# Kernel optimization log

Hardware: AMD Instinct MI355X
Metric: run time of the kernel (lower is better)

## Reference

```python
import jax, jax.numpy as jnp
import numpy as np

# Dimensions chosen per init_kwargs / input_specs
B, INC, OUTC, H, W = 16, 512, 256, 32, 32
FD = H * W           # flattened_dim = 1024 (perfect square)
DK = INC // 4        # 128, projection dim of the rotatory attention
EPS_BN = 1e-5


def setup_inputs() -> dict:
    key = jax.random.key(0)
    ks = jax.random.split(key, 8)
    sc = lambda fan_in: 1.0 / np.sqrt(fan_in)
    return {
        "x": jax.random.normal(ks[0], (B, INC, H, W), jnp.float32),
        "s": jax.random.normal(ks[1], (B, OUTC, 2 * H, 2 * W), jnp.float32),
        # ConvTranspose2d(inc, outc, 2, 2): torch weight shape (in, out, kH, kW)
        "up_w": jax.random.normal(ks[2], (INC, OUTC, 2, 2), jnp.float32) * sc(INC * 4),
        "up_b": jnp.zeros((OUTC,), jnp.float32),
        # LinearRotatoryAttentionModule projections: Linear(flattened_dim, inc//4) x3
        "wq": jax.random.normal(ks[3], (FD, DK), jnp.float32) * sc(FD),
        "wkl": jax.random.normal(ks[4], (FD, DK), jnp.float32) * sc(FD),
        "wkr": jax.random.normal(ks[5], (FD, DK), jnp.float32) * sc(FD),
        # conv_block(2*outc, outc): Conv2d 3x3 pad 1 + BatchNorm + ReLU
        "c1_w": jax.random.normal(ks[6], (OUTC, 2 * OUTC, 3, 3), jnp.float32) * sc(2 * OUTC * 9),
        "c1_b": jnp.zeros((OUTC,), jnp.float32),
        "bn_g": jnp.ones((OUTC,), jnp.float32),
        "bn_b": jnp.zeros((OUTC,), jnp.float32),
    }


def _rotatory(l, x, r, wq, wkl, wkr):
    """Linear rotatory attention on one triplet of slices, each (INC, FD).
    Center queries left and right contexts via elu+1 linear attention."""
    phi = lambda t: jax.nn.elu(t) + 1.0
    q = phi(x @ wq)        # (N, Dk)
    kl = phi(l @ wkl)      # (N, Dk)
    kr = phi(r @ wkr)      # (N, Dk)

    def linattn(k, v):
        kv = jnp.einsum('nk,nd->kd', k, v)      # (Dk, D)
        z = q @ k.sum(0) + 1e-6                  # (N,)
        return (q @ kv) / z[:, None]             # (N, D)

    return x + linattn(kl, l) + linattn(kr, r)


def reference(x, s, up_w, up_b, wq, wkl, wkr, c1_w, c1_b, bn_g, bn_b):
    # --- rotatory attention over interior batch samples (vectorized, no Python loop) ---
    xf = x.reshape(B, INC, FD)
    mid = jax.vmap(_rotatory, in_axes=(0, 0, 0, None, None, None))(
        xf[:-2], xf[1:-1], xf[2:], wq, wkl, wkr)          # (B-2, INC, FD)
    new = jnp.concatenate([x[:1], mid.reshape(B - 2, INC, H, W), x[-1:]], axis=0)

    # --- ConvTranspose2d k=2 s=2: non-overlapping, exact as einsum + reshape ---
    up = jnp.einsum('ncij,coab->noiajb', new, up_w).reshape(B, OUTC, 2 * H, 2 * W)
    up = up + up_b[None, :, None, None]

    # --- fused gate: sigmoid(relu(up + s)), then channel concat with skip ---
    g = jax.nn.sigmoid(jax.nn.relu(up + s))
    cat = jnp.concatenate([g, s], axis=1)                  # (B, 2*OUTC, 2H, 2W)

    # --- conv_block: Conv 3x3 same + BatchNorm (batch stats) + ReLU ---
    y = jax.lax.conv_general_dilated(cat, c1_w, (1, 1), 'SAME',
                                     dimension_numbers=('NCHW', 'OIHW', 'NCHW'))
    y = y + c1_b[None, :, None, None]
    mu = y.mean(axis=(0, 2, 3), keepdims=True)
    var = y.var(axis=(0, 2, 3), keepdims=True)
    y = (y - mu) / jnp.sqrt(var + EPS_BN)
    y = y * bn_g[None, :, None, None] + bn_b[None, :, None, None]
    return jax.nn.relu(y)
```

## Files before the change

### kernel.cpp

```cpp
#include <hip/hip_runtime.h>
#include <math.h>

#define B_ 16
#define INC 512
#define OUTC 256
#define FD 1024
#define DK 128
#define T_ 14
#define HO 64
#define WO 64
#define SP (HO*WO)
#define KC5P 40

typedef unsigned short u16;
typedef __attribute__((ext_vector_type(8))) short shortx8;
typedef __attribute__((ext_vector_type(4))) float floatx4;

__device__ __forceinline__ float phi_f(float t) {
    return t > 0.0f ? t + 1.0f : expf(t);
}
__device__ __forceinline__ u16 f2bf(float f) {
    unsigned int u = __float_as_uint(f);
    unsigned int r = (u + 0x7fffu + ((u >> 16) & 1u)) >> 16;
    return (u16)r;
}
__device__ __forceinline__ float bf2f(u16 h) {
    return __uint_as_float(((unsigned int)h) << 16);
}

__global__ __launch_bounds__(256) void kprep_x(const float* __restrict__ x, u16* __restrict__ xT) {
    __shared__ u16 T[64][65];
    int d0 = blockIdx.x * 64, c0 = blockIdx.y * 64, b = blockIdx.z;
    const float* src = x + (size_t)b * INC * FD;
    int tid = threadIdx.x, lr = tid >> 6, lc = tid & 63;
    #pragma unroll
    for (int i = 0; i < 16; ++i) {
        int c = lr + i * 4;
        T[lc][c] = f2bf(src[(size_t)(c0 + c) * FD + d0 + lc]);
    }
    __syncthreads();
    u16* dst = xT + (size_t)b * FD * INC;
    #pragma unroll
    for (int i = 0; i < 16; ++i) {
        int d = lr + i * 4;
        dst[(size_t)(d0 + d) * INC + c0 + lc] = T[d][lc];
    }
}

__global__ __launch_bounds__(256) void ktr_w(const float* __restrict__ src, u16* __restrict__ dst,
                                             int R, int C) {
    __shared__ u16 T[64][65];
    int c0 = blockIdx.x * 64, r0 = blockIdx.y * 64;
    int tid = threadIdx.x, lr = tid >> 6, lc = tid & 63;
    #pragma unroll
    for (int i = 0; i < 16; ++i) {
        int r = lr + i * 4;
        T[lc][r] = f2bf(src[(size_t)(r0 + r) * C + c0 + lc]);
    }
    __syncthreads();
    #pragma unroll
    for (int i = 0; i < 16; ++i) {
        int c = lr + i * 4;
        dst[(size_t)(c0 + c) * R + r0 + lc] = T[c][lc];
    }
}

__global__ void kw_tr(const float* __restrict__ c1_w, u16* __restrict__ Wt) {
    int i = blockIdx.x * 256 + threadIdx.x;
    if (i >= 256 * 512 * 9) return;
    int tap = i % 9; int t2 = i / 9;
    int c = t2 % 512; int o = t2 / 512;
    Wt[((size_t)tap * 256 + o) * 512 + c] = f2bf(c1_w[i]);
}

__global__ __launch_bounds__(256) void kborder(u16* __restrict__ P) {
    int b = blockIdx.y;
    int cbase = blockIdx.x * 20;
    uint4 z = {0, 0, 0, 0};
    for (int i = threadIdx.x; i < 20 * 64; i += 256) {
        int c = cbase + (i >> 6);
        int sub = i & 63;
        int row, col;
        if (c < 66)       { row = 0;       col = c; }
        else if (c < 132) { row = 65;      col = c - 66; }
        else if (c < 196) { row = c - 131; col = 0; }
        else              { row = c - 195; col = 65; }
        *(uint4*)(P + ((size_t)(b * 66 + row) * 66 + col) * 512 + sub * 8) = z;
    }
}

__global__ __launch_bounds__(256) void k1_proj(const float* __restrict__ x,
        const u16* __restrict__ wqT, const u16* __restrict__ wklT, const u16* __restrict__ wkrT,
        u16* __restrict__ qb, u16* __restrict__ klt, u16* __restrict__ krt) {
    __shared__ u16 smem[8704];
    u16* As = smem;
    u16* Bs = smem + 5120;
    int z = blockIdx.z, t = z / 3, which = z - t * 3;
    int src = (which == 0) ? t + 1 : (which == 1 ? t : t + 2);
    const float* Af = x + (size_t)src * INC * FD;
    const u16* Bw = (which == 0) ? wqT : (which == 1 ? wklT : wkrT);
    int n0 = blockIdx.x * 64, m0 = blockIdx.y * 128;
    int tid = threadIdx.x, w = tid >> 6, lane = tid & 63, l15 = lane & 15, quad = lane >> 4;
    int sm = tid >> 2, sq = (tid & 3) * 8;
    floatx4 acc[2][4];
    #pragma unroll
    for (int i = 0; i < 2; ++i)
        #pragma unroll
        for (int j = 0; j < 4; ++j) acc[i][j] = (floatx4){0.f,0.f,0.f,0.f};

    for (int k0 = 0; k0 < FD; k0 += 32) {
        float4 v0 = *(const float4*)&Af[(size_t)(m0 + sm) * FD + k0 + sq];
        float4 v1 = *(const float4*)&Af[(size_t)(m0 + sm) * FD + k0 + sq + 4];
        float4 v2 = *(const float4*)&Af[(size_t)(m0 + 64 + sm) * FD + k0 + sq];
        float4 v3 = *(const float4*)&Af[(size_t)(m0 + 64 + sm) * FD + k0 + sq + 4];
        union { u16 h[8]; uint4 v; } p0, p1;
        p0.h[0]=f2bf(v0.x); p0.h[1]=f2bf(v0.y); p0.h[2]=f2bf(v0.z); p0.h[3]=f2bf(v0.w);
        p0.h[4]=f2bf(v1.x); p0.h[5]=f2bf(v1.y); p0.h[6]=f2bf(v1.z); p0.h[7]=f2bf(v1.w);
        p1.h[0]=f2bf(v2.x); p1.h[1]=f2bf(v2.y); p1.h[2]=f2bf(v2.z); p1.h[3]=f2bf(v2.w);
        p1.h[4]=f2bf(v3.x); p1.h[5]=f2bf(v3.y); p1.h[6]=f2bf(v3.z); p1.h[7]=f2bf(v3.w);
        *(uint4*)&As[sm * 40 + sq] = p0.v;
        *(uint4*)&As[(64 + sm) * 40 + sq] = p1.v;
        *(uint4*)&Bs[sm * 40 + sq] = *(const uint4*)&Bw[(size_t)(n0 + sm) * FD + k0 + sq];
        __syncthreads();
        shortx8 bfr[4];
        #pragma unroll
        for (int nt = 0; nt < 4; ++nt)
            bfr[nt] = *(const shortx8*)&Bs[(nt * 16 + l15) * 40 + quad * 8];
        #pragma unroll
        for (int mt = 0; mt < 2; ++mt) {
            shortx8 af = *(const shortx8*)&As[(w * 32 + mt * 16 + l15) * 40 + quad * 8];
            #pragma unroll
            for (int nt = 0; nt < 4; ++nt)
                acc[mt][nt] = __builtin_amdgcn_mfma_f32_16x16x32_bf16(af, bfr[nt], acc[mt][nt], 0, 0, 0);
        }
        __syncthreads();
    }
    if (which == 0) {
        u16* outp = qb + (size_t)t * INC * DK;
        #pragma unroll
        for (int mt = 0; mt < 2; ++mt)
            #pragma unroll
            for (int nt = 0; nt < 4; ++nt)
                #pragma unroll
                for (int r = 0; r < 4; ++r) {
                    int m_out = m0 + w * 32 + mt * 16 + quad * 4 + r;
                    int n_out = n0 + nt * 16 + l15;
                    outp[(size_t)m_out * DK + n_out] = f2bf(phi_f(acc[mt][nt][r]));
                }
    } else {
        u16* outp = ((which == 1) ? klt : krt) + (size_t)t * DK * INC;
        #pragma unroll
        for (int mt = 0; mt < 2; ++mt)
            #pragma unroll
            for (int nt = 0; nt < 4; ++nt)
                #pragma unroll
                for (int r = 0; r < 4; ++r) {
                    int mloc = w * 32 + mt * 16 + quad * 4 + r;
                    int nloc = nt * 16 + l15;
                    smem[nloc * 136 + mloc] = f2bf(phi_f(acc[mt][nt][r]));
                }
        __syncthreads();
        int dkl = tid >> 2, seg = tid & 3;
        const uint4* sp = (const uint4*)&smem[dkl * 136 + seg * 32];
        uint4* dp = (uint4*)&outp[(size_t)(n0 + dkl) * INC + m0 + seg * 32];
        dp[0] = sp[0]; dp[1] = sp[1]; dp[2] = sp[2]; dp[3] = sp[3];
    }
}

__global__ __launch_bounds__(128) void k2b_ksum(const u16* __restrict__ klt, const u16* __restrict__ krt,
                         float* __restrict__ ksuml, float* __restrict__ ksumr) {
    int t = blockIdx.x, nb = blockIdx.y;
    int dk = threadIdx.x;
    const u16* pl = klt + ((size_t)t * DK + dk) * INC + nb * 64;
    const u16* pr = krt + ((size_t)t * DK + dk) * INC + nb * 64;
    float s1 = 0.f, s2 = 0.f;
    #pragma unroll
    for (int i = 0; i < 8; ++i) {
        union { uint4 v; u16 h[8]; } a, b;
        a.v = *(const uint4*)(pl + i * 8);
        b.v = *(const uint4*)(pr + i * 8);
        #pragma unroll
        for (int e = 0; e < 8; ++e) { s1 += bf2f(a.h[e]); s2 += bf2f(b.h[e]); }
    }
    atomicAdd(&ksuml[t * DK + dk], s1);
    atomicAdd(&ksumr[t * DK + dk], s2);
}

__global__ __launch_bounds__(512) void k2c_z(const u16* __restrict__ qb, const float* __restrict__ ksuml,
                      const float* __restrict__ ksumr, float* __restrict__ zl, float* __restrict__ zr) {
    int t = blockIdx.x; int n = threadIdx.x;
    const uint4* qp = (const uint4*)(qb + ((size_t)t * INC + n) * DK);
    const float* sl = ksuml + t * DK;
    const float* sr = ksumr + t * DK;
    float a = 0.f, b = 0.f;
    #pragma unroll
    for (int k16 = 0; k16 < 16; ++k16) {
        union { uint4 v; u16 h[8]; } q;
        q.v = qp[k16];
        #pragma unroll
        for (int e = 0; e < 8; ++e) {
            float qv = bf2f(q.h[e]);
            a = fmaf(qv, sl[k16 * 8 + e], a);
            b = fmaf(qv, sr[k16 * 8 + e], b);
        }
    }
    zl[t * INC + n] = a + 1e-6f;
    zr[t * INC + n] = b + 1e-6f;
}

__global__ __launch_bounds__(256) void k2_kv(const u16* __restrict__ xT,
        const u16* __restrict__ klt, const u16* __restrict__ krt,
        u16* __restrict__ kvlT, u16* __restrict__ kvrT) {
    __shared__ u16 As[128 * 40];
    __shared__ u16 Bs[64 * 40];
    int z = blockIdx.z, t = z >> 1, side = z & 1;
    const u16* A = xT + (size_t)(side ? t + 2 : t) * FD * INC;
    const u16* Bw = (side ? krt : klt) + (size_t)t * DK * INC;
    u16* outp = (side ? kvrT : kvlT) + (size_t)t * FD * DK;
    int n0 = blockIdx.x * 64, m0 = blockIdx.y * 128;
    int tid = threadIdx.x, w = tid >> 6, lane = tid & 63, l15 = lane & 15, quad = lane >> 4;
    int sm = tid >> 2, sq = (tid & 3) * 8;
    floatx4 acc[2][4];
    #pragma unroll
    for (int i = 0; i < 2; ++i)
        #pragma unroll
        for (int j = 0; j < 4; ++j) acc[i][j] = (floatx4){0.f,0.f,0.f,0.f};
    for (int k0 = 0; k0 < INC; k0 += 32) {
        *(uint4*)&As[sm * 40 + sq] = *(const uint4*)&A[(size_t)(m0 + sm) * INC + k0 + sq];
        *(uint4*)&As[(64 + sm) * 40 + sq] = *(const uint4*)&A[(size_t)(m0 + 64 + sm) * INC + k0 + sq];
        *(uint4*)&Bs[sm * 40 + sq] = *(const uint4*)&Bw[(size_t)(n0 + sm) * INC + k0 + sq];
        __syncthreads();
        shortx8 bfr[4];
        #pragma unroll
        for (int nt = 0; nt < 4; ++nt)
            bfr[nt] = *(const shortx8*)&Bs[(nt * 16 + l15) * 40 + quad * 8];
        #pragma unroll
        for (int mt = 0; mt < 2; ++mt) {
            shortx8 af = *(const shortx8*)&As[(w * 32 + mt * 16 + l15) * 40 + quad * 8];
            #pragma unroll
            for (int nt = 0; nt < 4; ++nt)
                acc[mt][nt] = __builtin_amdgcn_mfma_f32_16x16x32_bf16(af, bfr[nt], acc[mt][nt], 0, 0, 0);
        }
        __syncthreads();
    }
    #pragma unroll
    for (int mt = 0; mt < 2; ++mt)
        #pragma unroll
        for (int nt = 0; nt < 4; ++nt)
            #pragma unroll
            for (int r = 0; r < 4; ++r) {
                int m_out = m0 + w * 32 + mt * 16 + quad * 4 + r;
                int n_out = n0 + nt * 16 + l15;
                outp[(size_t)m_out * DK + n_out] = f2bf(acc[mt][nt][r]);
            }
}

__global__ __launch_bounds__(256) void k3_out(const u16* __restrict__ xT,
        const u16* __restrict__ qb, const u16* __restrict__ kvlT, const u16* __restrict__ kvrT,
        const float* __restrict__ zl, const float* __restrict__ zr, u16* __restrict__ newT) {
    __shared__ u16 As1[128 * 40];
    __shared__ u16 As2[128 * 40];
    __shared__ u16 Bs[64 * 40];
    int t = blockIdx.z;
    const u16* A1 = kvlT + (size_t)t * FD * DK;
    const u16* A2 = kvrT + (size_t)t * FD * DK;
    const u16* Bq = qb + (size_t)t * INC * DK;
    int n0 = blockIdx.x * 64, m0 = blockIdx.y * 128;
    int tid = threadIdx.x, w = tid >> 6, lane = tid & 63, l15 = lane & 15, quad = lane >> 4;
    int sm = tid >> 2, sq = (tid & 3) * 8;
    floatx4 accl[2][4], accr[2][4];
    #pragma unroll
    for (int i = 0; i < 2; ++i)
        #pragma unroll
        for (int j = 0; j < 4; ++j) {
            accl[i][j] = (floatx4){0.f,0.f,0.f,0.f};
            accr[i][j] = (floatx4){0.f,0.f,0.f,0.f};
        }
    for (int k0 = 0; k0 < DK; k0 += 32) {
        *(uint4*)&As1[sm * 40 + sq] = *(const uint4*)&A1[(size_t)(m0 + sm) * DK + k0 + sq];
        *(uint4*)&As1[(64 + sm) * 40 + sq] = *(const uint4*)&A1[(size_t)(m0 + 64 + sm) * DK + k0 + sq];
        *(uint4*)&As2[sm * 40 + sq] = *(const uint4*)&A2[(size_t)(m0 + sm) * DK + k0 + sq];
        *(uint4*)&As2[(64 + sm) * 40 + sq] = *(const uint4*)&A2[(size_t)(m0 + 64 + sm) * DK + k0 + sq];
        *(uint4*)&Bs[sm * 40 + sq] = *(const uint4*)&Bq[(size_t)(n0 + sm) * DK + k0 + sq];
        __syncthreads();
        shortx8 bfr[4];
        #pragma unroll
        for (int nt = 0; nt < 4; ++nt)
            bfr[nt] = *(const shortx8*)&Bs[(nt * 16 + l15) * 40 + quad * 8];
        #pragma unroll
        for (int mt = 0; mt < 2; ++mt) {
            shortx8 afl = *(const shortx8*)&As1[(w * 32 + mt * 16 + l15) * 40 + quad * 8];
            shortx8 afr = *(const shortx8*)&As2[(w * 32 + mt * 16 + l15) * 40 + quad * 8];
            #pragma unroll
            for (int nt = 0; nt < 4; ++nt) {
                accl[mt][nt] = __builtin_amdgcn_mfma_f32_16x16x32_bf16(afl, bfr[nt], accl[mt][nt], 0, 0, 0);
                accr[mt][nt] = __builtin_amdgcn_mfma_f32_16x16x32_bf16(afr, bfr[nt], accr[mt][nt], 0, 0, 0);
            }
        }
        __syncthreads();
    }
    float il[4], ir[4];
    #pragma unroll
    for (int nt = 0; nt < 4; ++nt) {
        int n_out = n0 + nt * 16 + l15;
        il[nt] = 1.0f / zl[t * INC + n_out];
        ir[nt] = 1.0f / zr[t * INC + n_out];
    }
    const u16* xc = xT + (size_t)(t + 1) * FD * INC;
    u16* outp = newT + (size_t)t * FD * INC;
    #pragma unroll
    for (int mt = 0; mt < 2; ++mt)
        #pragma unroll
        for (int nt = 0; nt < 4; ++nt)
            #pragma unroll
            for (int r = 0; r < 4; ++r) {
                int m_out = m0 + w * 32 + mt * 16 + quad * 4 + r;
                int n_out = n0 + nt * 16 + l15;
                float xv = bf2f(xc[(size_t)m_out * INC + n_out]);
                float v = xv + accl[mt][nt][r] * il[nt] + accr[mt][nt][r] * ir[nt];
                outp[(size_t)m_out * INC + n_out] = f2bf(v);
            }
}

__global__ __launch_bounds__(256) void k4_up(const u16* __restrict__ xT,
        const u16* __restrict__ newT, const u16* __restrict__ upwT,
        const float* __restrict__ up_b, u16* __restrict__ P) {
    __shared__ u16 smem[12288];
    u16* As = smem;
    u16* Bs = smem + 5120;
    int b = blockIdx.z;
    const u16* A = (b == 0) ? xT
                 : (b == B_ - 1) ? (xT + (size_t)(B_ - 1) * FD * INC)
                 : (newT + (size_t)(b - 1) * FD * INC);
    int n0 = blockIdx.x * 64, m0 = blockIdx.y * 128;
    int tid = threadIdx.x, w = tid >> 6, lane = tid & 63, l15 = lane & 15, quad = lane >> 4;
    int sm = tid >> 2, sq = (tid & 3) * 8;
    floatx4 acc[2][4];
    #pragma unroll
    for (int i = 0; i < 2; ++i)
        #pragma unroll
        for (int j = 0; j < 4; ++j) acc[i][j] = (floatx4){0.f,0.f,0.f,0.f};
    for (int k0 = 0; k0 < INC; k0 += 32) {
        *(uint4*)&As[sm * 40 + sq] = *(const uint4*)&A[(size_t)(m0 + sm) * INC + k0 + sq];
        *(uint4*)&As[(64 + sm) * 40 + sq] = *(const uint4*)&A[(size_t)(m0 + 64 + sm) * INC + k0 + sq];
        *(uint4*)&Bs[sm * 40 + sq] = *(const uint4*)&upwT[(size_t)(n0 + sm) * INC + k0 + sq];
        __syncthreads();
        shortx8 bfr[4];
        #pragma unroll
        for (int nt = 0; nt < 4; ++nt)
            bfr[nt] = *(const shortx8*)&Bs[(nt * 16 + l15) * 40 + quad * 8];
        #pragma unroll
        for (int mt = 0; mt < 2; ++mt) {
            shortx8 af = *(const shortx8*)&As[(w * 32 + mt * 16 + l15) * 40 + quad * 8];
            #pragma unroll
            for (int nt = 0; nt < 4; ++nt)
                acc[mt][nt] = __builtin_amdgcn_mfma_f32_16x16x32_bf16(af, bfr[nt], acc[mt][nt], 0, 0, 0);
        }
        __syncthreads();
    }
    u16* Ts = smem;
    int ppos = (l15 & 3) * 128;
    #pragma unroll
    for (int mt = 0; mt < 2; ++mt)
        #pragma unroll
        for (int nt = 0; nt < 4; ++nt) {
            int lm = nt * 16 + l15;
            float bias = up_b[(n0 + lm) >> 2];
            int o_rel = lm >> 2;
            #pragma unroll
            for (int r = 0; r < 4; ++r) {
                int l = w * 32 + mt * 16 + quad * 4 + r;
                Ts[(ppos + l) * 24 + o_rel] = f2bf(acc[mt][nt][r] + bias);
            }
        }
    __syncthreads();
    #pragma unroll
    for (int j2 = 0; j2 < 2; ++j2) {
        int pi = tid + j2 * 256;
        int pp = pi >> 7, l = pi & 127;
        int aa = pp >> 1, cbb = pp & 1;
        int px = m0 + l;
        int row = 2 * (px >> 5) + aa, colq = 2 * (px & 31) + cbb;
        size_t dst = ((size_t)(b * 66 + 1 + row) * 66 + 1 + colq) * 512 + (n0 >> 2);
        union { uint4 v; u16 h[8]; } a0, a1, s0, s1, g0, g1;
        a0.v = *(const uint4*)&Ts[pi * 24];
        a1.v = *(const uint4*)&Ts[pi * 24 + 8];
        s0.v = *(const uint4*)(P + dst + 256);
        s1.v = *(const uint4*)(P + dst + 256 + 8);
        #pragma unroll
        for (int e = 0; e < 8; ++e) {
            float r0 = fmaxf(bf2f(a0.h[e]) + bf2f(s0.h[e]), 0.0f);
            float r1 = fmaxf(bf2f(a1.h[e]) + bf2f(s1.h[e]), 0.0f);
            g0.h[e] = f2bf(1.0f / (1.0f + expf(-r0)));
            g1.h[e] = f2bf(1.0f / (1.0f + expf(-r1)));
        }
        *(uint4*)(P + dst) = g0.v;
        *(uint4*)(P + dst + 8) = g1.v;
    }
}

__global__ __launch_bounds__(256) void k4b_sfill(const float* __restrict__ s_in,
                                                 u16* __restrict__ P) {
    __shared__ u16 T[64 * 264];
    int p = blockIdx.x;
    int b = blockIdx.y;
    int tid = threadIdx.x;
    int qcol = tid & 63;
    int ob = tid >> 6;
    for (int o = ob; o < 256; o += 4) {
        float v = s_in[((size_t)(b * OUTC + o) * HO + p) * WO + qcol];
        T[qcol * 264 + o] = f2bf(v);
    }
    __syncthreads();
    int q2 = tid >> 2;
    int sg = tid & 3;
    size_t base = ((size_t)(b * 66 + 1 + p) * 66 + 1 + q2) * 512 + 256;
    #pragma unroll
    for (int it = 0; it < 8; ++it) {
        int seg = sg + it * 4;
        uint4 v = *(const uint4*)&T[q2 * 264 + seg * 8];
        *(uint4*)(P + base + seg * 8) = v;
    }
}

__global__ __launch_bounds__(256) void k5_mfma(const u16* __restrict__ P,
        const u16* __restrict__ Wt, const float* __restrict__ c1_b,
        float* __restrict__ y) {
    __shared__ u16 Xs[6 * 66 * KC5P];
    int rb = blockIdx.x;
    int o0 = blockIdx.y * 64;
    int b  = blockIdx.z;
    int tid = threadIdx.x;
    int w = tid >> 6, lane = tid & 63;
    int l15 = lane & 15, quad = lane >> 4;

    floatx4 acc[4][4];
    #pragma unroll
    for (int i = 0; i < 4; ++i)
        #pragma unroll
        for (int j = 0; j < 4; ++j)
            acc[i][j] = (floatx4){0.f, 0.f, 0.f, 0.f};

    size_t Pbase = ((size_t)b * 66 + (size_t)rb * 4) * 66 * 512;
    const u16* Wbase = Wt + ((size_t)o0 + (size_t)l15) * 512 + quad * 8;

    for (int ch = 0; ch < 16; ++ch) {
        int c0 = ch * 32;
        __syncthreads();
        #pragma unroll
        for (int it = 0; it < 8; ++it) {
            int s = it * 256 + tid;
            if (s < 1980) {
                int pix = s / 5;
                int cs = s - pix * 5;
                int csel = (cs == 4) ? 0 : cs;
                const u16* gp = P + Pbase + (size_t)pix * 512 + c0 + csel * 8;
                __builtin_amdgcn_global_load_lds(
                    (const __attribute__((address_space(1))) void*)gp,
                    (__attribute__((address_space(3))) void*)&Xs[(size_t)(it * 256 + w * 64) * 8],
                    16, 0, 0);
            }
        }
        __syncthreads();
        shortx8 wfb[2][4];
        #pragma unroll
        for (int nt = 0; nt < 4; ++nt)
            wfb[0][nt] = *(const shortx8*)(Wbase + ((size_t)nt * 16) * 512 + c0);
        #pragma unroll
        for (int tap = 0; tap < 9; ++tap) {
            if (tap < 8) {
                #pragma unroll
                for (int nt = 0; nt < 4; ++nt)
                    wfb[(tap + 1) & 1][nt] = *(const shortx8*)(Wbase +
                        ((size_t)(tap + 1) * 256 + (size_t)nt * 16) * 512 + c0);
            }
            int dy = tap / 3, dx = tap - dy * 3;
            #pragma unroll
            for (int mt = 0; mt < 4; ++mt) {
                shortx8 af = *(const shortx8*)&Xs[((w + dy) * 66 + mt * 16 + l15 + dx) * KC5P + quad * 8];
                #pragma unroll
                for (int nt = 0; nt < 4; ++nt)
                    acc[mt][nt] = __builtin_amdgcn_mfma_f32_16x16x32_bf16(
                        af, wfb[tap & 1][nt], acc[mt][nt], 0, 0, 0);
            }
        }
    }
    int row = rb * 4 + w;
    float bias[4];
    #pragma unroll
    for (int nt = 0; nt < 4; ++nt) bias[nt] = c1_b[o0 + nt * 16 + l15];
    #pragma unroll
    for (int mt = 0; mt < 4; ++mt) {
        #pragma unroll
        for (int nt = 0; nt < 4; ++nt) {
            int o = o0 + nt * 16 + l15;
            size_t ybase = (size_t)(b * OUTC + o) * SP + row * 64;
            float4 v;
            v.x = acc[mt][nt][0] + bias[nt];
            v.y = acc[mt][nt][1] + bias[nt];
            v.z = acc[mt][nt][2] + bias[nt];
            v.w = acc[mt][nt][3] + bias[nt];
            *(float4*)&y[ybase + mt * 16 + quad * 4] = v;
        }
    }
}

__global__ __launch_bounds__(256) void k6_bnred(const float* __restrict__ y,
        float* __restrict__ bnsum, float* __restrict__ bnsq) {
    int b = blockIdx.x, o = blockIdx.y;
    const float* p = y + ((size_t)b * OUTC + o) * SP;
    float s1 = 0.f, s2 = 0.f;
    for (int i = threadIdx.x; i < SP; i += 256) { float v = p[i]; s1 += v; s2 = fmaf(v, v, s2); }
    #pragma unroll
    for (int off = 32; off > 0; off >>= 1) {
        s1 += __shfl_down(s1, off, 64);
        s2 += __shfl_down(s2, off, 64);
    }
    __shared__ float r1[4], r2[4];
    int wid = threadIdx.x >> 6, lane = threadIdx.x & 63;
    if (lane == 0) { r1[wid] = s1; r2[wid] = s2; }
    __syncthreads();
    if (threadIdx.x == 0) {
        atomicAdd(&bnsum[o], r1[0] + r1[1] + r1[2] + r1[3]);
        atomicAdd(&bnsq[o],  r2[0] + r2[1] + r2[2] + r2[3]);
    }
}

__global__ void k7_bnfin(const float* __restrict__ bnsum, const float* __restrict__ bnsq,
                         const float* __restrict__ bn_g, const float* __restrict__ bn_b,
                         float* __restrict__ scale, float* __restrict__ shift) {
    int o = threadIdx.x;
    float cnt = (float)(B_ * SP);
    float mu = bnsum[o] / cnt;
    float var = bnsq[o] / cnt - mu * mu;
    float sc = bn_g[o] * rsqrtf(var + 1e-5f);
    scale[o] = sc;
    shift[o] = bn_b[o] - mu * sc;
}

__global__ __launch_bounds__(256) void k8_apply(float* __restrict__ y,
        const float* __restrict__ scale, const float* __restrict__ shift) {
    int i = blockIdx.x * 256 + threadIdx.x;
    int o = (i >> 10) & 255;
    float4 v = ((float4*)y)[i];
    float sc = scale[o], sh = shift[o];
    v.x = fmaxf(fmaf(v.x, sc, sh), 0.f);
    v.y = fmaxf(fmaf(v.y, sc, sh), 0.f);
    v.z = fmaxf(fmaf(v.z, sc, sh), 0.f);
    v.w = fmaxf(fmaf(v.w, sc, sh), 0.f);
    ((float4*)y)[i] = v;
}

extern "C" void kernel_launch(void* const* d_in, const int* in_sizes, int n_in,
                              void* d_out, int out_size, void* d_ws, size_t ws_size,
                              hipStream_t stream) {
    const float* x    = (const float*)d_in[0];
    const float* s_in = (const float*)d_in[1];
    const float* up_w = (const float*)d_in[2];
    const float* up_b = (const float*)d_in[3];
    const float* wq   = (const float*)d_in[4];
    const float* wkl  = (const float*)d_in[5];
    const float* wkr  = (const float*)d_in[6];
    const float* c1_w = (const float*)d_in[7];
    const float* c1_b = (const float*)d_in[8];
    const float* bn_g = (const float*)d_in[9];
    const float* bn_b = (const float*)d_in[10];
    float* y = (float*)d_out;
    float* ws = (float*)d_ws;

    size_t off = 0;
    float* bnsum = ws + off; off += OUTC;
    float* bnsq  = ws + off; off += OUTC;
    float* ksuml = ws + off; off += (size_t)T_ * DK;
    float* ksumr = ws + off; off += (size_t)T_ * DK;
    float* zl    = ws + off; off += (size_t)T_ * INC;
    float* zr    = ws + off; off += (size_t)T_ * INC;
    float* scale = ws + off; off += OUTC;
    float* shift = ws + off; off += OUTC;

    u16* ub = (u16*)(ws + off);
    size_t uo = 0;
    u16* qb   = ub + uo; uo += (size_t)T_ * INC * DK;
    u16* klt  = ub + uo; uo += (size_t)T_ * DK * INC;
    u16* krt  = ub + uo; uo += (size_t)T_ * DK * INC;
    u16* kvlT = ub + uo; uo += (size_t)T_ * FD * DK;
    u16* kvrT = ub + uo; uo += (size_t)T_ * FD * DK;
    u16* newT = ub + uo; uo += (size_t)T_ * FD * INC;
    u16* xT   = ub + uo; uo += (size_t)B_ * FD * INC;
    u16* wqT  = ub + uo; uo += (size_t)DK * FD;
    u16* wklT = ub + uo; uo += (size_t)DK * FD;
    u16* wkrT = ub + uo; uo += (size_t)DK * FD;
    u16* upwT = ub + uo; uo += (size_t)FD * INC;
    u16* Wt   = ub + uo; uo += (size_t)9 * OUTC * 2 * INC;
    u16* P    = ub + uo; uo += (size_t)B_ * 66 * 66 * 512;

    hipMemsetAsync(bnsum, 0, (2 * OUTC + 2 * T_ * DK) * sizeof(float), stream);

    kborder<<<dim3(13, B_), dim3(256), 0, stream>>>(P);
    kprep_x<<<dim3(16, 8, B_), dim3(256), 0, stream>>>(x, xT);
    ktr_w<<<dim3(2, 16), dim3(256), 0, stream>>>(wq, wqT, FD, DK);
    ktr_w<<<dim3(2, 16), dim3(256), 0, stream>>>(wkl, wklT, FD, DK);
    ktr_w<<<dim3(2, 16), dim3(256), 0, stream>>>(wkr, wkrT, FD, DK);
    ktr_w<<<dim3(16, 8), dim3(256), 0, stream>>>(up_w, upwT, INC, FD);
    kw_tr<<<dim3((256 * 512 * 9 + 255) / 256), dim3(256), 0, stream>>>(c1_w, Wt);

    k1_proj<<<dim3(2, 4, 42), dim3(256), 0, stream>>>(x, wqT, wklT, wkrT, qb, klt, krt);
    k2b_ksum<<<dim3(T_, 8), dim3(128), 0, stream>>>(klt, krt, ksuml, ksumr);
    k2c_z<<<dim3(T_), dim3(512), 0, stream>>>(qb, ksuml, ksumr, zl, zr);
    k2_kv<<<dim3(2, 8, 28), dim3(256), 0, stream>>>(xT, klt, krt, kvlT, kvrT);
    k3_out<<<dim3(8, 8, T_), dim3(256), 0, stream>>>(xT, qb, kvlT, kvrT, zl, zr, newT);
    k4b_sfill<<<dim3(64, B_), dim3(256), 0, stream>>>(s_in, P);
    k4_up<<<dim3(16, 8, B_), dim3(256), 0, stream>>>(xT, newT, upwT, up_b, P);
    k5_mfma<<<dim3(16, 4, B_), dim3(256), 0, stream>>>(P, Wt, c1_b, y);
    k6_bnred<<<dim3(B_, OUTC), dim3(256), 0, stream>>>(y, bnsum, bnsq);
    k7_bnfin<<<dim3(1), dim3(OUTC), 0, stream>>>(bnsum, bnsq, bn_g, bn_b, scale, shift);
    k8_apply<<<dim3((B_ * OUTC * SP / 4) / 256), dim3(256), 0, stream>>>(y, scale, shift);
}
```

Before: 681.4 us.

## Double-buffer conv LDS tiles, widen output tile, fuse BN reduction into conv

The 3x3 conv MFMA kernel now double-buffers its input-channel chunks in LDS, issuing the next chunk's global-to-LDS loads before computing the current one. It also prefetches weight fragments across chunk boundaries. Each block now computes 128 output channels instead of 64, which halves the grid and doubles accumulator registers. The BatchNorm sum and sum-of-squares reduction moves into the conv epilogue using shuffles and atomics, removing the separate k6 pass that re-read y. The LDS row padding is dropped to fit two buffers, which may add bank conflicts, and the larger register footprint may lower occupancy.

```diff
diff --git a/kernel.cpp b/kernel.cpp
--- a/kernel.cpp
+++ b/kernel.cpp
@@ -10,7 +10,7 @@
 #define HO 64
 #define WO 64
 #define SP (HO*WO)
-#define KC5P 40
+#define KC5 32
 
 typedef unsigned short u16;
 typedef __attribute__((ext_vector_type(8))) short shortx8;
@@ -423,106 +423,115 @@
     }
 }
 
-__global__ __launch_bounds__(256) void k5_mfma(const u16* __restrict__ P,
+__global__ __launch_bounds__(256, 2) void k5_mfma(const u16* __restrict__ P,
         const u16* __restrict__ Wt, const float* __restrict__ c1_b,
-        float* __restrict__ y) {
-    __shared__ u16 Xs[6 * 66 * KC5P];
+        float* __restrict__ y, float* __restrict__ bnsum, float* __restrict__ bnsq) {
+    __shared__ u16 Xs[2][6 * 66 * KC5];
     int rb = blockIdx.x;
-    int o0 = blockIdx.y * 64;
+    int o0 = blockIdx.y * 128;
     int b  = blockIdx.z;
     int tid = threadIdx.x;
     int w = tid >> 6, lane = tid & 63;
     int l15 = lane & 15, quad = lane >> 4;
 
-    floatx4 acc[4][4];
+    floatx4 acc[4][8];
     #pragma unroll
     for (int i = 0; i < 4; ++i)
         #pragma unroll
-        for (int j = 0; j < 4; ++j)
+        for (int j = 0; j < 8; ++j)
             acc[i][j] = (floatx4){0.f, 0.f, 0.f, 0.f};
 
     size_t Pbase = ((size_t)b * 66 + (size_t)rb * 4) * 66 * 512;
-    const u16* Wbase = Wt + ((size_t)o0 + (size_t)l15) * 512 + quad * 8;
+    const u16* Wbase = Wt + ((size_t)(o0 + l15)) * 512 + quad * 8;
+
+    #pragma unroll
+    for (int it = 0; it < 7; ++it) {
+        int s = it * 256 + tid;
+        if (s < 1584) {
+            int pix = s >> 2, cs = s & 3;
+            const u16* gp = P + Pbase + (size_t)pix * 512 + cs * 8;
+            __builtin_amdgcn_global_load_lds(
+                (const __attribute__((address_space(1))) void*)gp,
+                (__attribute__((address_space(3))) void*)&Xs[0][(size_t)(it * 256 + w * 64) * 8],
+                16, 0, 0);
+        }
+    }
+    shortx8 wfb[2][8];
+    #pragma unroll
+    for (int nt = 0; nt < 8; ++nt)
+        wfb[0][nt] = *(const shortx8*)(Wbase + ((size_t)nt * 16) * 512);
 
     for (int ch = 0; ch < 16; ++ch) {
         int c0 = ch * 32;
         __syncthreads();
-        #pragma unroll
-        for (int it = 0; it < 8; ++it) {
-            int s = it * 256 + tid;
-            if (s < 1980) {
-                int pix = s / 5;
-                int cs = s - pix * 5;
-                int csel = (cs == 4) ? 0 : cs;
-                const u16* gp = P + Pbase + (size_t)pix * 512 + c0 + csel * 8;
-                __builtin_amdgcn_global_load_lds(
-                    (const __attribute__((address_space(1))) void*)gp,
-                    (__attribute__((address_space(3))) void*)&Xs[(size_t)(it * 256 + w * 64) * 8],
-                    16, 0, 0);
+        if (ch < 15) {
+            int c1 = c0 + 32;
+            int nb = (ch + 1) & 1;
+            #pragma unroll
+            for (int it = 0; it < 7; ++it) {
+                int s = it * 256 + tid;
+                if (s < 1584) {
+                    int pix = s >> 2, cs = s & 3;
+                    const u16* gp = P + Pbase + (size_t)pix * 512 + c1 + cs * 8;
+                    __builtin_amdgcn_global_load_lds(
+                        (const __attribute__((address_space(1))) void*)gp,
+                        (__attribute__((address_space(3))) void*)&Xs[nb][(size_t)(it * 256 + w * 64) * 8],
+                        16, 0, 0);
+                }
             }
         }
-        __syncthreads();
-        shortx8 wfb[2][4];
-        #pragma unroll
-        for (int nt = 0; nt < 4; ++nt)
-            wfb[0][nt] = *(const shortx8*)(Wbase + ((size_t)nt * 16) * 512 + c0);
+        const u16* xb = Xs[ch & 1];
         #pragma unroll
         for (int tap = 0; tap < 9; ++tap) {
+            int wsel = (ch + tap) & 1;
             if (tap < 8) {
                 #pragma unroll
-                for (int nt = 0; nt < 4; ++nt)
-                    wfb[(tap + 1) & 1][nt] = *(const shortx8*)(Wbase +
-                        ((size_t)(tap + 1) * 256 + (size_t)nt * 16) * 512 + c0);
+                for (int nt = 0; nt < 8; ++nt)
+                    wfb[wsel ^ 1][nt] = *(const shortx8*)(Wbase +
+                        ((size_t)((tap + 1) * 256 + nt * 16)) * 512 + c0);
+            } else if (ch < 15) {
+                #pragma unroll
+                for (int nt = 0; nt < 8; ++nt)
+                    wfb[wsel ^ 1][nt] = *(const shortx8*)(Wbase +
+                        ((size_t)(nt * 16)) * 512 + c0 + 32);
             }
             int dy = tap / 3, dx = tap - dy * 3;
             #pragma unroll
             for (int mt = 0; mt < 4; ++mt) {
-                shortx8 af = *(const shortx8*)&Xs[((w + dy) * 66 + mt * 16 + l15 + dx) * KC5P + quad * 8];
+                shortx8 af = *(const shortx8*)&xb[((w + dy) * 66 + mt * 16 + l15 + dx) * KC5 + quad * 8];
                 #pragma unroll
-                for (int nt = 0; nt < 4; ++nt)
+                for (int nt = 0; nt < 8; ++nt)
                     acc[mt][nt] = __builtin_amdgcn_mfma_f32_16x16x32_bf16(
-                        af, wfb[tap & 1][nt], acc[mt][nt], 0, 0, 0);
+                        af, wfb[wsel][nt], acc[mt][nt], 0, 0, 0);
             }
         }
     }
     int row = rb * 4 + w;
-    float bias[4];
-    #pragma unroll
-    for (int nt = 0; nt < 4; ++nt) bias[nt] = c1_b[o0 + nt * 16 + l15];
-    #pragma unroll
-    for (int mt = 0; mt < 4; ++mt) {
-        #pragma unroll
-        for (int nt = 0; nt < 4; ++nt) {
-            int o = o0 + nt * 16 + l15;
-            size_t ybase = (size_t)(b * OUTC + o) * SP + row * 64;
+    #pragma unroll
+    for (int nt = 0; nt < 8; ++nt) {
+        int o = o0 + nt * 16 + l15;
+        float bias = c1_b[o];
+        float s1 = 0.f, s2 = 0.f;
+        size_t ybase = (size_t)(b * OUTC + o) * SP + row * 64;
+        #pragma unroll
+        for (int mt = 0; mt < 4; ++mt) {
             float4 v;
-            v.x = acc[mt][nt][0] + bias[nt];
-            v.y = acc[mt][nt][1] + bias[nt];
-            v.z = acc[mt][nt][2] + bias[nt];
-            v.w = acc[mt][nt][3] + bias[nt];
+            v.x = acc[mt][nt][0] + bias;
+            v.y = acc[mt][nt][1] + bias;
+            v.z = acc[mt][nt][2] + bias;
+            v.w = acc[mt][nt][3] + bias;
             *(float4*)&y[ybase + mt * 16 + quad * 4] = v;
-        }
-    }
-}
-
-__global__ __launch_bounds__(256) void k6_bnred(const float* __restrict__ y,
-        float* __restrict__ bnsum, float* __restrict__ bnsq) {
-    int b = blockIdx.x, o = blockIdx.y;
-    const float* p = y + ((size_t)b * OUTC + o) * SP;
-    float s1 = 0.f, s2 = 0.f;
-    for (int i = threadIdx.x; i < SP; i += 256) { float v = p[i]; s1 += v; s2 = fmaf(v, v, s2); }
-    #pragma unroll
-    for (int off = 32; off > 0; off >>= 1) {
-        s1 += __shfl_down(s1, off, 64);
-        s2 += __shfl_down(s2, off, 64);
-    }
-    __shared__ float r1[4], r2[4];
-    int wid = threadIdx.x >> 6, lane = threadIdx.x & 63;
-    if (lane == 0) { r1[wid] = s1; r2[wid] = s2; }
-    __syncthreads();
-    if (threadIdx.x == 0) {
-        atomicAdd(&bnsum[o], r1[0] + r1[1] + r1[2] + r1[3]);
-        atomicAdd(&bnsq[o],  r2[0] + r2[1] + r2[2] + r2[3]);
+            s1 += v.x + v.y + v.z + v.w;
+            s2 += v.x * v.x + v.y * v.y + v.z * v.z + v.w * v.w;
+        }
+        s1 += __shfl_xor(s1, 16);
+        s1 += __shfl_xor(s1, 32);
+        s2 += __shfl_xor(s2, 16);
+        s2 += __shfl_xor(s2, 32);
+        if (quad == 0) {
+            atomicAdd(&bnsum[o], s1);
+            atomicAdd(&bnsq[o], s2);
+        }
     }
 }
 
@@ -611,8 +620,7 @@
     k3_out<<<dim3(8, 8, T_), dim3(256), 0, stream>>>(xT, qb, kvlT, kvrT, zl, zr, newT);
     k4b_sfill<<<dim3(64, B_), dim3(256), 0, stream>>>(s_in, P);
     k4_up<<<dim3(16, 8, B_), dim3(256), 0, stream>>>(xT, newT, upwT, up_b, P);
-    k5_mfma<<<dim3(16, 4, B_), dim3(256), 0, stream>>>(P, Wt, c1_b, y);
-    k6_bnred<<<dim3(B_, OUTC), dim3(256), 0, stream>>>(y, bnsum, bnsq);
+    k5_mfma<<<dim3(16, 2, B_), dim3(256), 0, stream>>>(P, Wt, c1_b, y, bnsum, bnsq);
     k7_bnfin<<<dim3(1), dim3(OUTC), 0, stream>>>(bnsum, bnsq, bn_g, bn_b, scale, shift);
     k8_apply<<<dim3((B_ * OUTC * SP / 4) / 256), dim3(256), 0, stream>>>(y, scale, shift);
 }
```

New measurement: 1.032 ms. +51.4%, slower.
